# Optimization experiments

Hardware: AMD Instinct MI355X
Metric: run time of the kernel (lower is better)

## Reference

```python
import jax, jax.numpy as jnp
import numpy as np


def setup_inputs() -> dict:
    key = jax.random.key(0)
    k1, k2, k3, k4, k5 = jax.random.split(key, 5)
    B, D, H, W, C = 2, 16, 16, 16, 256
    x = jax.random.normal(k1, (B, D, H, W, C), dtype=jnp.float32)
    Wf = jax.random.normal(k2, (C, C // 4), dtype=jnp.float32) * (1.0 / np.sqrt(C))
    Wg = jax.random.normal(k3, (C, C // 4), dtype=jnp.float32) * (1.0 / np.sqrt(C))
    Wh = jax.random.normal(k4, (C, C), dtype=jnp.float32) * (1.0 / np.sqrt(C))
    gamma = jax.random.normal(k5, (1,), dtype=jnp.float32) * 0.1
    return {"x": x, "Wf": Wf, "Wg": Wg, "Wh": Wh, "gamma": gamma}


def reference(x, Wf, Wg, Wh, gamma):
    B, D, H, W, C = x.shape
    N = D * H * W
    xf = x.reshape(B, N, C)  # hw_flatten of input (1x1x1 conv == per-position matmul)
    f = jnp.einsum('bnc,cf->bnf', xf, Wf)   # [B, N, C//4]
    g = jnp.einsum('bnc,cf->bnf', xf, Wg)   # [B, N, C//4]
    h = jnp.einsum('bnc,cf->bnf', xf, Wh)   # [B, N, C]
    s = jnp.einsum('bnf,bmf->bnm', g, f)    # g @ f^T, [B, N, N]
    beta = jax.nn.softmax(s, axis=-1)
    o = jnp.einsum('bnm,bmc->bnc', beta, h)  # [B, N, C]
    out = gamma * o.reshape(B, D, H, W, C) + x
    beta_out = beta.reshape(-1, D, H, W, 1)  # [B*N, D, H, W, 1] as in original
    return (out, beta_out)
```

## Files before the change

### kernel.cpp

```cpp
#include <hip/hip_runtime.h>

#define NPOS 4096
#define CDIM 256
#define FDIM 64

typedef short short8 __attribute__((ext_vector_type(8)));
typedef float f32x4 __attribute__((ext_vector_type(4)));

__device__ __forceinline__ unsigned short f2bf(float v) {
  unsigned u = __float_as_uint(v);
  unsigned r = (u + 0x7fffu + ((u >> 16) & 1u)) >> 16;
  return (unsigned short)r;
}
__device__ __forceinline__ float bf2f(unsigned short u) {
  return __uint_as_float((unsigned)u << 16);
}
__device__ __forceinline__ short8 as_s8(uint4 u) {
  return *reinterpret_cast<short8*>(&u);
}
__device__ __forceinline__ void gload_lds16(const void* g, void* l) {
  __builtin_amdgcn_global_load_lds(
      (const __attribute__((address_space(1))) unsigned int*)g,
      (__attribute__((address_space(3))) unsigned int*)l, 16, 0, 0);
}

__global__ __launch_bounds__(256) void proj_kernel(
    const float* __restrict__ x, const float* __restrict__ Wf,
    const float* __restrict__ Wg, const float* __restrict__ Wh,
    unsigned short* __restrict__ f_hi, unsigned short* __restrict__ f_lo,
    unsigned short* __restrict__ g_hi, unsigned short* __restrict__ g_lo,
    unsigned short* __restrict__ h_t, float* __restrict__ out) {
  __shared__ float xs[16][CDIM];
  const int row0 = blockIdx.x * 16;
  const int t = threadIdx.x;
  {
    const float4* xv = reinterpret_cast<const float4*>(x + (size_t)row0 * CDIM);
    float4* sv = reinterpret_cast<float4*>(&xs[0][0]);
    float4* ov = reinterpret_cast<float4*>(out + (size_t)row0 * CDIM);
#pragma unroll
    for (int i = 0; i < 4; ++i) {
      const float4 v = xv[t + 256 * i];
      sv[t + 256 * i] = v;
      ov[t + 256 * i] = v;
    }
  }
  __syncthreads();
  {
    float acc[16];
#pragma unroll
    for (int r = 0; r < 16; ++r) acc[r] = 0.f;
    for (int k = 0; k < CDIM; k += 4) {
      const float w0 = Wh[(size_t)(k + 0) * CDIM + t];
      const float w1 = Wh[(size_t)(k + 1) * CDIM + t];
      const float w2 = Wh[(size_t)(k + 2) * CDIM + t];
      const float w3 = Wh[(size_t)(k + 3) * CDIM + t];
#pragma unroll
      for (int r = 0; r < 16; ++r) {
        const float4 xv = *reinterpret_cast<const float4*>(&xs[r][k]);
        float a = acc[r];
        a = fmaf(xv.x, w0, a);
        a = fmaf(xv.y, w1, a);
        a = fmaf(xv.z, w2, a);
        a = fmaf(xv.w, w3, a);
        acc[r] = a;
      }
    }
    const int b = row0 >> 12;
    const int lr = row0 & (NPOS - 1);
    unsigned wd[8];
#pragma unroll
    for (int i = 0; i < 8; ++i)
      wd[i] = (unsigned)f2bf(acc[2 * i]) | ((unsigned)f2bf(acc[2 * i + 1]) << 16);
    uint4* base = reinterpret_cast<uint4*>(h_t + ((size_t)(b * CDIM + t)) * NPOS);
    const int m = t & 7;
    const int c0 = lr >> 3;
    base[c0 ^ m] = make_uint4(wd[0], wd[1], wd[2], wd[3]);
    base[(c0 + 1) ^ m] = make_uint4(wd[4], wd[5], wd[6], wd[7]);
  }
  {
    const int col = t & 63;
    const int rb = (t >> 6) * 4;
    const int colq = col >> 3, cwi = col & 7;
    float af[4] = {0.f, 0.f, 0.f, 0.f};
    float ag[4] = {0.f, 0.f, 0.f, 0.f};
    for (int k = 0; k < CDIM; k += 4) {
      const float wf0 = Wf[(size_t)(k + 0) * FDIM + col];
      const float wf1 = Wf[(size_t)(k + 1) * FDIM + col];
      const float wf2 = Wf[(size_t)(k + 2) * FDIM + col];
      const float wf3 = Wf[(size_t)(k + 3) * FDIM + col];
      const float wg0 = Wg[(size_t)(k + 0) * FDIM + col];
      const float wg1 = Wg[(size_t)(k + 1) * FDIM + col];
      const float wg2 = Wg[(size_t)(k + 2) * FDIM + col];
      const float wg3 = Wg[(size_t)(k + 3) * FDIM + col];
#pragma unroll
      for (int r = 0; r < 4; ++r) {
        const float4 xv = *reinterpret_cast<const float4*>(&xs[rb + r][k]);
        float a = af[r], bb = ag[r];
        a = fmaf(xv.x, wf0, a); a = fmaf(xv.y, wf1, a);
        a = fmaf(xv.z, wf2, a); a = fmaf(xv.w, wf3, a);
        bb = fmaf(xv.x, wg0, bb); bb = fmaf(xv.y, wg1, bb);
        bb = fmaf(xv.z, wg2, bb); bb = fmaf(xv.w, wg3, bb);
        af[r] = a; ag[r] = bb;
      }
    }
#pragma unroll
    for (int r = 0; r < 4; ++r) {
      const int row = row0 + rb + r;
      const int ph = ((colq ^ (row & 7)) << 3) | cwi;
      const size_t of = (size_t)row * FDIM + ph;
      const size_t og = (size_t)row * FDIM + col;
      const unsigned short fh = f2bf(af[r]);
      const unsigned short gh = f2bf(ag[r]);
      f_hi[of] = fh;
      f_lo[of] = f2bf(af[r] - bf2f(fh));
      g_hi[og] = gh;
      g_lo[og] = f2bf(ag[r] - bf2f(gh));
    }
  }
}

__global__ __launch_bounds__(1024, 4) void qk_l_kernel(
    const unsigned short* __restrict__ f_hi, const unsigned short* __restrict__ f_lo,
    const unsigned short* __restrict__ g_hi, const unsigned short* __restrict__ g_lo,
    unsigned short* __restrict__ Pws, float* __restrict__ lrow) {
  __shared__ uint4 Fh[2][256][8];
  __shared__ uint4 Fl[2][256][8];
  __shared__ float partl[16][32];

  const int wg = blockIdx.x;
  const int wgid = (wg & 7) * 32 + (wg >> 3);
  const int b = wgid >> 7;
  const int row0 = (wgid & 127) * 32;
  const int t = threadIdx.x;
  const int w = t >> 6;
  const int l = t & 63;
  const int lr = l & 15;
  const int lk = l >> 4;

  short8 gh0[2], gl0[2], gh1[2], gl1[2];
  {
    const unsigned short* gH0 = g_hi + ((size_t)(b * NPOS + row0 + lr)) * FDIM + lk * 8;
    const unsigned short* gL0 = g_lo + ((size_t)(b * NPOS + row0 + lr)) * FDIM + lk * 8;
    const unsigned short* gH1 = gH0 + (size_t)16 * FDIM;
    const unsigned short* gL1 = gL0 + (size_t)16 * FDIM;
#pragma unroll
    for (int ks = 0; ks < 2; ++ks) {
      gh0[ks] = *reinterpret_cast<const short8*>(gH0 + ks * 32);
      gl0[ks] = *reinterpret_cast<const short8*>(gL0 + ks * 32);
      gh1[ks] = *reinterpret_cast<const short8*>(gH1 + ks * 32);
      gl1[ks] = *reinterpret_cast<const short8*>(gL1 + ks * 32);
    }
  }
  const unsigned short* fbh = f_hi + (size_t)b * NPOS * FDIM;
  const unsigned short* fbl = f_lo + (size_t)b * NPOS * FDIM;
  unsigned short* prow0 = Pws + (size_t)(b * NPOS + row0 + lr) * NPOS;
  unsigned short* prow1 = prow0 + (size_t)16 * NPOS;
  const int rsw = lr & 7;
  float lsum0 = 0.f, lsum1 = 0.f;

#define STAGEA(buf, tile)                                                      \
  do {                                                                         \
    _Pragma("unroll")                                                          \
    for (int j = 0; j < 2; ++j) {                                              \
      const int slot_ = j * 1024 + t;                                          \
      const int row_ = slot_ >> 3, ch_ = slot_ & 7;                            \
      gload_lds16(fbh + (size_t)((tile) * 256 + row_) * FDIM + ch_ * 8,        \
                  (char*)&Fh[buf][0][0] + (size_t)slot_ * 16);                 \
      gload_lds16(fbl + (size_t)((tile) * 256 + row_) * FDIM + ch_ * 8,        \
                  (char*)&Fl[buf][0][0] + (size_t)slot_ * 16);                 \
    }                                                                          \
  } while (0)

  STAGEA(0, 0);
  asm volatile("s_waitcnt vmcnt(0) lgkmcnt(0)\ns_barrier" ::: "memory");

  const int rrA = w * 16 + lr;
  const int fsw = rrA & 7;
  int buf = 0;
  for (int tile = 0; tile < 16; ++tile) {
    if (tile < 15) STAGEA(buf ^ 1, tile + 1);
    __builtin_amdgcn_sched_barrier(0);
    const uint4 h0 = Fh[buf][rrA][lk ^ fsw];
    const uint4 h1 = Fh[buf][rrA][(lk + 4) ^ fsw];
    const uint4 q0 = Fl[buf][rrA][lk ^ fsw];
    const uint4 q1 = Fl[buf][rrA][(lk + 4) ^ fsw];
    {
      f32x4 acca = {0.f, 0.f, 0.f, 0.f};
      f32x4 accb = {0.f, 0.f, 0.f, 0.f};
      acca = __builtin_amdgcn_mfma_f32_16x16x32_bf16(as_s8(h0), gh0[0], acca, 0, 0, 0);
      accb = __builtin_amdgcn_mfma_f32_16x16x32_bf16(as_s8(h0), gl0[0], accb, 0, 0, 0);
      acca = __builtin_amdgcn_mfma_f32_16x16x32_bf16(as_s8(q0), gh0[0], acca, 0, 0, 0);
      accb = __builtin_amdgcn_mfma_f32_16x16x32_bf16(as_s8(h1), gh0[1], accb, 0, 0, 0);
      acca = __builtin_amdgcn_mfma_f32_16x16x32_bf16(as_s8(q1), gh0[1], acca, 0, 0, 0);
      accb = __builtin_amdgcn_mfma_f32_16x16x32_bf16(as_s8(h1), gl0[1], accb, 0, 0, 0);
      const f32x4 acc = acca + accb;
      const int cq = tile * 256 + w * 16 + lk * 4;
      const float e0 = __expf(acc[0]);
      const float e1 = __expf(acc[1]);
      const float e2 = __expf(acc[2]);
      const float e3 = __expf(acc[3]);
      lsum0 += (e0 + e1) + (e2 + e3);
      uint2 pk;
      pk.x = (unsigned)f2bf(e0) | ((unsigned)f2bf(e1) << 16);
      pk.y = (unsigned)f2bf(e2) | ((unsigned)f2bf(e3) << 16);
      const int sidx = (((cq >> 3) ^ rsw) << 3) | (cq & 7);
      *reinterpret_cast<uint2*>(prow0 + sidx) = pk;
    }
    {
      f32x4 acca = {0.f, 0.f, 0.f, 0.f};
      f32x4 accb = {0.f, 0.f, 0.f, 0.f};
      acca = __builtin_amdgcn_mfma_f32_16x16x32_bf16(as_s8(h0), gh1[0], acca, 0, 0, 0);
      accb = __builtin_amdgcn_mfma_f32_16x16x32_bf16(as_s8(h0), gl1[0], accb, 0, 0, 0);
      acca = __builtin_amdgcn_mfma_f32_16x16x32_bf16(as_s8(q0), gh1[0], acca, 0, 0, 0);
      accb = __builtin_amdgcn_mfma_f32_16x16x32_bf16(as_s8(h1), gh1[1], accb, 0, 0, 0);
      acca = __builtin_amdgcn_mfma_f32_16x16x32_bf16(as_s8(q1), gh1[1], acca, 0, 0, 0);
      accb = __builtin_amdgcn_mfma_f32_16x16x32_bf16(as_s8(h1), gl1[1], accb, 0, 0, 0);
      const f32x4 acc = acca + accb;
      const int cq = tile * 256 + w * 16 + lk * 4;
      const float e0 = __expf(acc[0]);
      const float e1 = __expf(acc[1]);
      const float e2 = __expf(acc[2]);
      const float e3 = __expf(acc[3]);
      lsum1 += (e0 + e1) + (e2 + e3);
      uint2 pk;
      pk.x = (unsigned)f2bf(e0) | ((unsigned)f2bf(e1) << 16);
      pk.y = (unsigned)f2bf(e2) | ((unsigned)f2bf(e3) << 16);
      const int sidx = (((cq >> 3) ^ rsw) << 3) | (cq & 7);
      *reinterpret_cast<uint2*>(prow1 + sidx) = pk;
    }
    asm volatile("s_waitcnt vmcnt(2) lgkmcnt(0)\ns_barrier" ::: "memory");
    buf ^= 1;
  }
#undef STAGEA

  lsum0 += __shfl_xor(lsum0, 16);
  lsum0 += __shfl_xor(lsum0, 32);
  lsum1 += __shfl_xor(lsum1, 16);
  lsum1 += __shfl_xor(lsum1, 32);
  if (l < 16) {
    partl[w][l] = lsum0;
    partl[w][16 + l] = lsum1;
  }
  __syncthreads();
  if (t < 32) {
    float s = 0.f;
#pragma unroll
    for (int q = 0; q < 16; ++q) s += partl[q][t];
    lrow[(size_t)b * NPOS + row0 + t] = s;
  }
}

__global__ __launch_bounds__(1024, 4) void pv_split_kernel(
    const unsigned short* __restrict__ h_t, const unsigned short* __restrict__ Pws,
    const float* __restrict__ lrow, const float* __restrict__ gamma,
    float* __restrict__ beta, float* __restrict__ out) {
  __shared__ uint4 Ab[2][64][8];
  __shared__ uint4 Bb[2][256][8];
  __shared__ float linvB[64];

  const int wg = blockIdx.x;
  const int wgid = (wg & 7) * 32 + (wg >> 3);
  const int b = wgid >> 7;
  const int khalf = (wgid >> 6) & 1;
  const int row0 = (wgid & 63) * 64;
  const int t = threadIdx.x;
  const int w = t >> 6;
  const int l = t & 63;
  const int lr = l & 15;
  const int lk = l >> 4;

  if (t < 64) linvB[t] = __frcp_rn(lrow[(size_t)b * NPOS + row0 + t]);

  const size_t hoff = (size_t)b * CDIM * NPOS;
  const unsigned short* Pb = Pws + (size_t)(b * NPOS + row0) * NPOS;
  const int kbase = khalf * 256;

#define STAGEB(bufi, kt)                                                        \
  do {                                                                          \
    _Pragma("unroll")                                                           \
    for (int j = 0; j < 2; ++j) {                                               \
      const int slot_ = j * 1024 + t;                                           \
      const int col_ = slot_ >> 3, ch_ = slot_ & 7;                             \
      const unsigned short* g_ = h_t + hoff + (size_t)col_ * NPOS +             \
                                 (size_t)(kbase + (kt) * 8 + ch_) * 8;          \
      gload_lds16(g_, (char*)&Bb[bufi][0][0] + (size_t)slot_ * 16);             \
    }                                                                           \
    if (t < 512) {                                                              \
      const int row_ = t >> 3, ch_ = t & 7;                                     \
      const unsigned short* g_ = Pb + (size_t)row_ * NPOS +                     \
                                 (size_t)(kbase + (kt) * 8 + ch_) * 8;          \
      gload_lds16(g_, (char*)&Ab[bufi][0][0] + (size_t)t * 16);                 \
    }                                                                           \
  } while (0)

  f32x4 acc0 = {0.f, 0.f, 0.f, 0.f}, acc1 = {0.f, 0.f, 0.f, 0.f};
  f32x4 acc2 = {0.f, 0.f, 0.f, 0.f}, acc3 = {0.f, 0.f, 0.f, 0.f};
  const int wrB = w & 3;
  const int wcB = w >> 2;
  const int arB = wrB * 16 + lr;
  const int c0 = wcB * 64 + lr;
  const int c1 = c0 + 16;
  const int c2 = c0 + 32;
  const int c3 = c0 + 48;
  const int brow = t >> 4;
  const int jj = t & 15;

  STAGEB(0, 0);
  asm volatile("s_waitcnt vmcnt(0) lgkmcnt(0)\ns_barrier" ::: "memory");
  const float il_brow = linvB[brow];

  int buf = 0;
  for (int kt = 0; kt < 32; ++kt) {
    if (kt < 31) STAGEB(buf ^ 1, kt + 1);
    __builtin_amdgcn_sched_barrier(0);
    {
      const uint4 a0 = Ab[buf][arB][lk ^ (arB & 7)];
      const uint4 a1 = Ab[buf][arB][(4 + lk) ^ (arB & 7)];
      const uint4 b00 = Bb[buf][c0][lk ^ (c0 & 7)];
      const uint4 b01 = Bb[buf][c1][lk ^ (c1 & 7)];
      const uint4 b02 = Bb[buf][c2][lk ^ (c2 & 7)];
      const uint4 b03 = Bb[buf][c3][lk ^ (c3 & 7)];
      acc0 = __builtin_amdgcn_mfma_f32_16x16x32_bf16(as_s8(a0), as_s8(b00), acc0, 0, 0, 0);
      acc1 = __builtin_amdgcn_mfma_f32_16x16x32_bf16(as_s8(a0), as_s8(b01), acc1, 0, 0, 0);
      acc2 = __builtin_amdgcn_mfma_f32_16x16x32_bf16(as_s8(a0), as_s8(b02), acc2, 0, 0, 0);
      acc3 = __builtin_amdgcn_mfma_f32_16x16x32_bf16(as_s8(a0), as_s8(b03), acc3, 0, 0, 0);
      const uint4 b10 = Bb[buf][c0][(4 + lk) ^ (c0 & 7)];
      const uint4 b11 = Bb[buf][c1][(4 + lk) ^ (c1 & 7)];
      const uint4 b12 = Bb[buf][c2][(4 + lk) ^ (c2 & 7)];
      const uint4 b13 = Bb[buf][c3][(4 + lk) ^ (c3 & 7)];
      acc0 = __builtin_amdgcn_mfma_f32_16x16x32_bf16(as_s8(a1), as_s8(b10), acc0, 0, 0, 0);
      acc1 = __builtin_amdgcn_mfma_f32_16x16x32_bf16(as_s8(a1), as_s8(b11), acc1, 0, 0, 0);
      acc2 = __builtin_amdgcn_mfma_f32_16x16x32_bf16(as_s8(a1), as_s8(b12), acc2, 0, 0, 0);
      acc3 = __builtin_amdgcn_mfma_f32_16x16x32_bf16(as_s8(a1), as_s8(b13), acc3, 0, 0, 0);
    }
    {
      const uint4 u4 = Ab[buf][brow][(jj >> 1) ^ (brow & 7)];
      const uint2 u = (jj & 1) ? make_uint2(u4.z, u4.w) : make_uint2(u4.x, u4.y);
      float4 v;
      v.x = bf2f((unsigned short)(u.x & 0xffffu)) * il_brow;
      v.y = bf2f((unsigned short)(u.x >> 16)) * il_brow;
      v.z = bf2f((unsigned short)(u.y & 0xffffu)) * il_brow;
      v.w = bf2f((unsigned short)(u.y >> 16)) * il_brow;
      *reinterpret_cast<float4*>(beta + (size_t)(b * NPOS + row0 + brow) * NPOS +
                                 khalf * 2048 + kt * 64 + jj * 4) = v;
    }
    asm volatile("s_waitcnt vmcnt(1) lgkmcnt(0)\ns_barrier" ::: "memory");
    buf ^= 1;
  }
#undef STAGEB

  const float gam = gamma[0];
#pragma unroll
  for (int r = 0; r < 4; ++r) {
    const int lrr = wrB * 16 + lk * 4 + r;
    const int orow = row0 + lrr;
    const float sc = gam * linvB[lrr];
    float* o = out + ((size_t)b * NPOS + orow) * CDIM + wcB * 64 + lr;
    atomicAdd(o, sc * acc0[r]);
    atomicAdd(o + 16, sc * acc1[r]);
    atomicAdd(o + 32, sc * acc2[r]);
    atomicAdd(o + 48, sc * acc3[r]);
  }
}

__global__ __launch_bounds__(1024, 4) void attn_fused_kernel(
    const unsigned short* __restrict__ f_hi, const unsigned short* __restrict__ f_lo,
    const unsigned short* __restrict__ g_hi, const unsigned short* __restrict__ g_lo,
    const unsigned short* __restrict__ h_t, const float* __restrict__ x,
    const float* __restrict__ gamma, float* __restrict__ beta,
    float* __restrict__ out) {
  __shared__ __align__(16) char shraw[110592];
  __shared__ float partl[16][16];
  __shared__ float linvs[32];
  uint4 (*Fh)[128][8] = reinterpret_cast<uint4(*)[128][8]>(shraw);
  uint4 (*Fl)[128][8] = reinterpret_cast<uint4(*)[128][8]>(shraw + 32768);
  uint4 (*Ab)[32][8] = reinterpret_cast<uint4(*)[32][8]>(shraw);
  uint4 (*Bb)[256][8] = reinterpret_cast<uint4(*)[256][8]>(shraw + 12288);

  const int wg = blockIdx.x;
  const int wgid = (wg & 7) * 32 + (wg >> 3);
  const int b = wgid >> 7;
  const int row0 = (wgid & 127) * 32;
  const int t = threadIdx.x;
  const int w = t >> 6;
  const int l = t & 63;
  const int lr = l & 15;
  const int lk = l >> 4;

  const int wr = w >> 3;
  const int wq = w & 7;
  const int arow = row0 + wr * 16 + lr;
  short8 gh[2], gl[2];
  {
    const unsigned short* gH = g_hi + ((size_t)(b * NPOS + arow)) * FDIM + lk * 8;
    const unsigned short* gL = g_lo + ((size_t)(b * NPOS + arow)) * FDIM + lk * 8;
#pragma unroll
    for (int ks = 0; ks < 2; ++ks) {
      gh[ks] = *reinterpret_cast<const short8*>(gH + ks * 32);
      gl[ks] = *reinterpret_cast<const short8*>(gL + ks * 32);
    }
  }
  const unsigned short* fbh = f_hi + (size_t)b * NPOS * FDIM;
  const unsigned short* fbl = f_lo + (size_t)b * NPOS * FDIM;
  unsigned short* Pb = (unsigned short*)(beta + (size_t)b * NPOS * NPOS);
  unsigned short* prow = Pb + (size_t)arow * (2 * NPOS) + NPOS;
  const int rsw = lr & 7;
  float lsum = 0.f;
  const int srow_ = t >> 3, sch_ = t & 7;

#define STAGEA(buf, tile)                                                      \
  do {                                                                         \
    const int tr_ = (tile) * 128 + srow_;                                      \
    gload_lds16(fbh + (size_t)tr_ * FDIM + sch_ * 8,                           \
                (char*)&Fh[buf][0][0] + (size_t)t * 16);                       \
    gload_lds16(fbl + (size_t)tr_ * FDIM + sch_ * 8,                           \
                (char*)&Fl[buf][0][0] + (size_t)t * 16);                       \
  } while (0)

  STAGEA(0, 0);
  asm volatile("s_waitcnt vmcnt(0) lgkmcnt(0)\ns_barrier" ::: "memory");

  const int rrA = wq * 16 + lr;
  const int fsw = rrA & 7;
  int buf = 0;
  for (int tile = 0; tile < 32; ++tile) {
    if (tile < 31) STAGEA(buf ^ 1, tile + 1);
    __builtin_amdgcn_sched_barrier(0);
    const uint4 h0 = Fh[buf][rrA][lk ^ fsw];
    const uint4 h1 = Fh[buf][rrA][(lk + 4) ^ fsw];
    const uint4 q0 = Fl[buf][rrA][lk ^ fsw];
    const uint4 q1 = Fl[buf][rrA][(lk + 4) ^ fsw];
    f32x4 acca = {0.f, 0.f, 0.f, 0.f};
    f32x4 accb = {0.f, 0.f, 0.f, 0.f};
    acca = __builtin_amdgcn_mfma_f32_16x16x32_bf16(as_s8(h0), gh[0], acca, 0, 0, 0);
    accb = __builtin_amdgcn_mfma_f32_16x16x32_bf16(as_s8(h0), gl[0], accb, 0, 0, 0);
    acca = __builtin_amdgcn_mfma_f32_16x16x32_bf16(as_s8(q0), gh[0], acca, 0, 0, 0);
    accb = __builtin_amdgcn_mfma_f32_16x16x32_bf16(as_s8(h1), gh[1], accb, 0, 0, 0);
    acca = __builtin_amdgcn_mfma_f32_16x16x32_bf16(as_s8(q1), gh[1], acca, 0, 0, 0);
    accb = __builtin_amdgcn_mfma_f32_16x16x32_bf16(as_s8(h1), gl[1], accb, 0, 0, 0);
    const f32x4 acc = acca + accb;
    const int cq = tile * 128 + wq * 16 + lk * 4;
    const float e0 = __expf(acc[0]);
    const float e1 = __expf(acc[1]);
    const float e2 = __expf(acc[2]);
    const float e3 = __expf(acc[3]);
    lsum += (e0 + e1) + (e2 + e3);
    uint2 pk;
    pk.x = (unsigned)f2bf(e0) | ((unsigned)f2bf(e1) << 16);
    pk.y = (unsigned)f2bf(e2) | ((unsigned)f2bf(e3) << 16);
    const int sidx = (((cq >> 3) ^ rsw) << 3) | (cq & 7);
    *reinterpret_cast<uint2*>(prow + sidx) = pk;
    asm volatile("s_waitcnt vmcnt(1) lgkmcnt(0)\ns_barrier" ::: "memory");
    buf ^= 1;
  }
#undef STAGEA

  lsum += __shfl_xor(lsum, 16);
  lsum += __shfl_xor(lsum, 32);
  if (l < 16) partl[w][l] = lsum;
  __syncthreads();
  if (t < 32) {
    const int half = t >> 4;
    float s = 0.f;
#pragma unroll
    for (int q = 0; q < 8; ++q) s += partl[half * 8 + q][t & 15];
    linvs[t] = __frcp_rn(s);
  }
  asm volatile("s_waitcnt vmcnt(0) lgkmcnt(0)\ns_barrier" ::: "memory");

  const size_t hoff = (size_t)b * CDIM * NPOS;
  const unsigned short* Pub = (const unsigned short*)(beta + (size_t)b * NPOS * NPOS);

#define STAGEB(bufi, kt)                                                        \
  do {                                                                          \
    {                                                                           \
      const int slot_ = w * 128 + l;                                            \
      const unsigned short* g_ = h_t + hoff + (size_t)(slot_ >> 3) * NPOS +     \
                                 (size_t)((kt) * 8 + (slot_ & 7)) * 8;          \
      gload_lds16(g_, (unsigned short*)&Bb[bufi][0][0] + (size_t)(w * 128) * 8);\
    }                                                                           \
    {                                                                           \
      const int slot_ = w * 128 + 64 + l;                                       \
      const unsigned short* g_ = h_t + hoff + (size_t)(slot_ >> 3) * NPOS +     \
                                 (size_t)((kt) * 8 + (slot_ & 7)) * 8;          \
      gload_lds16(g_, (unsigned short*)&Bb[bufi][0][0] +                        \
                          (size_t)(w * 128 + 64) * 8);                          \
    }                                                                           \
    if (t < 256) {                                                              \
      const unsigned short* g_ = Pub + (size_t)(row0 + (t >> 3)) * (2 * NPOS) + \
                                 NPOS + (size_t)((kt) * 8 + (t & 7)) * 8;       \
      gload_lds16(g_, (unsigned short*)&Ab[bufi][0][0] + (size_t)(w * 64) * 8); \
    }                                                                           \
  } while (0)

  f32x4 acc0 = {0.f, 0.f, 0.f, 0.f}, acc1 = {0.f, 0.f, 0.f, 0.f};
  const int wrB = w & 1;
  const int wcB = w >> 1;
  const int arB = wrB * 16 + lr;
  const int c0 = wcB * 32 + lr;
  const int c1 = c0 + 16;
  const int brow = t >> 5;
  const int jj = t & 31;
  const float il_brow = linvs[brow];

  STAGEB(0, 0);
  asm volatile("s_waitcnt vmcnt(0) lgkmcnt(0)\ns_barrier" ::: "memory");

  buf = 0;
  for (int kt = 0; kt < 64; ++kt) {
    if (kt < 63) STAGEB(buf ^ 1, kt + 1);
    __builtin_amdgcn_sched_barrier(0);
    {
      const uint4 a0 = Ab[buf][arB][lk ^ (arB & 7)];
      const uint4 a1 = Ab[buf][arB][(4 + lk) ^ (arB & 7)];
      const uint4 b00 = Bb[buf][c0][lk ^ (c0 & 7)];
      const uint4 b01 = Bb[buf][c1][lk ^ (c1 & 7)];
      const uint4 b10 = Bb[buf][c0][(4 + lk) ^ (c0 & 7)];
      const uint4 b11 = Bb[buf][c1][(4 + lk) ^ (c1 & 7)];
      acc0 = __builtin_amdgcn_mfma_f32_16x16x32_bf16(as_s8(a0), as_s8(b00), acc0, 0, 0, 0);
      acc1 = __builtin_amdgcn_mfma_f32_16x16x32_bf16(as_s8(a0), as_s8(b01), acc1, 0, 0, 0);
      acc0 = __builtin_amdgcn_mfma_f32_16x16x32_bf16(as_s8(a1), as_s8(b10), acc0, 0, 0, 0);
      acc1 = __builtin_amdgcn_mfma_f32_16x16x32_bf16(as_s8(a1), as_s8(b11), acc1, 0, 0, 0);
    }
    {
      const unsigned* arow_ = reinterpret_cast<const unsigned*>(&Ab[buf][brow][0]);
      const unsigned u = arow_[(((jj >> 2) ^ (brow & 7)) << 2) | (jj & 3)];
      float2 v;
      v.x = bf2f((unsigned short)(u & 0xffffu)) * il_brow;
      v.y = bf2f((unsigned short)(u >> 16)) * il_brow;
      *reinterpret_cast<float2*>(beta + (size_t)(b * NPOS + row0 + brow) * NPOS +
                                 (size_t)kt * 64 + jj * 2) = v;
    }
    asm volatile("s_waitcnt vmcnt(1) lgkmcnt(0)\ns_barrier" ::: "memory");
    buf ^= 1;
  }
#undef STAGEB

  const float gam = gamma[0];
#pragma unroll
  for (int r = 0; r < 4; ++r) {
    const int lrr = wrB * 16 + lk * 4 + r;
    const int orow = row0 + lrr;
    const float sc = gam * linvs[lrr];
    const size_t i0 = ((size_t)b * NPOS + orow) * CDIM + wcB * 32 + lr;
    out[i0] = fmaf(sc, acc0[r], x[i0]);
    out[i0 + 16] = fmaf(sc, acc1[r], x[i0 + 16]);
  }
}

extern "C" void kernel_launch(void* const* d_in, const int* in_sizes, int n_in,
                              void* d_out, int out_size, void* d_ws, size_t ws_size,
                              hipStream_t stream) {
  (void)in_sizes; (void)n_in; (void)out_size;
  const float* x = (const float*)d_in[0];
  const float* Wf = (const float*)d_in[1];
  const float* Wg = (const float*)d_in[2];
  const float* Wh = (const float*)d_in[3];
  const float* gamma = (const float*)d_in[4];

  float* out = (float*)d_out;
  float* beta = out + (size_t)2 * NPOS * CDIM;

  unsigned short* h_t = (unsigned short*)d_ws;
  unsigned short* f_hi = h_t + (size_t)2 * CDIM * NPOS;
  unsigned short* f_lo = f_hi + (size_t)2 * NPOS * FDIM;
  unsigned short* g_hi = f_lo + (size_t)2 * NPOS * FDIM;
  unsigned short* g_lo = g_hi + (size_t)2 * NPOS * FDIM;
  float* lrow = (float*)(g_lo + (size_t)2 * NPOS * FDIM);
  unsigned short* Pws = (unsigned short*)(lrow + 2 * NPOS);

  const size_t need = ((char*)(Pws + (size_t)2 * NPOS * NPOS)) - (char*)d_ws;

  hipLaunchKernelGGL(proj_kernel, dim3(2 * NPOS / 16), dim3(256), 0, stream,
                     x, Wf, Wg, Wh, f_hi, f_lo, g_hi, g_lo, h_t, out);
  if (ws_size >= need) {
    hipLaunchKernelGGL(qk_l_kernel, dim3(256), dim3(1024), 0, stream,
                       f_hi, f_lo, g_hi, g_lo, Pws, lrow);
    hipLaunchKernelGGL(pv_split_kernel, dim3(256), dim3(1024), 0, stream,
                       h_t, Pws, lrow, gamma, beta, out);
  } else {
    hipLaunchKernelGGL(attn_fused_kernel, dim3(256), dim3(1024), 0, stream,
                       f_hi, f_lo, g_hi, g_lo, h_t, x, gamma, beta, out);
  }
}
```

Baseline: 125.7 us.

## Retile PV split kernel to 128-row blocks with four-way K split

Changes the PV kernel tiling so each workgroup handles 128 query rows against a quarter of the key range, instead of 64 rows against half. Each staged h tile is now reused by twice as many rows, and each wave computes eight accumulators instead of four, which cuts global traffic for h per unit of work. The cost is twice as many atomic partial-sum adds into the output, plus higher register and LDS use per block. The waitcnt is adjusted because each iteration now issues two beta stores.

```diff
diff --git a/kernel.cpp b/kernel.cpp
--- a/kernel.cpp
+++ b/kernel.cpp
@@ -254,26 +254,26 @@
     const unsigned short* __restrict__ h_t, const unsigned short* __restrict__ Pws,
     const float* __restrict__ lrow, const float* __restrict__ gamma,
     float* __restrict__ beta, float* __restrict__ out) {
-  __shared__ uint4 Ab[2][64][8];
+  __shared__ uint4 Ab[2][128][8];
   __shared__ uint4 Bb[2][256][8];
-  __shared__ float linvB[64];
+  __shared__ float linvB[128];
 
   const int wg = blockIdx.x;
   const int wgid = (wg & 7) * 32 + (wg >> 3);
   const int b = wgid >> 7;
-  const int khalf = (wgid >> 6) & 1;
-  const int row0 = (wgid & 63) * 64;
+  const int kq = (wgid >> 5) & 3;
+  const int row0 = (wgid & 31) * 128;
   const int t = threadIdx.x;
   const int w = t >> 6;
   const int l = t & 63;
   const int lr = l & 15;
   const int lk = l >> 4;
 
-  if (t < 64) linvB[t] = __frcp_rn(lrow[(size_t)b * NPOS + row0 + t]);
+  if (t < 128) linvB[t] = __frcp_rn(lrow[(size_t)b * NPOS + row0 + t]);
 
   const size_t hoff = (size_t)b * CDIM * NPOS;
   const unsigned short* Pb = Pws + (size_t)(b * NPOS + row0) * NPOS;
-  const int kbase = khalf * 256;
+  const int kbase = kq * 128;
 
 #define STAGEB(bufi, kt)                                                        \
   do {                                                                          \
@@ -285,7 +285,7 @@
                                  (size_t)(kbase + (kt) * 8 + ch_) * 8;          \
       gload_lds16(g_, (char*)&Bb[bufi][0][0] + (size_t)slot_ * 16);             \
     }                                                                           \
-    if (t < 512) {                                                              \
+    {                                                                           \
       const int row_ = t >> 3, ch_ = t & 7;                                     \
       const unsigned short* g_ = Pb + (size_t)row_ * NPOS +                     \
                                  (size_t)(kbase + (kt) * 8 + ch_) * 8;          \
@@ -293,47 +293,45 @@
     }                                                                           \
   } while (0)
 
-  f32x4 acc0 = {0.f, 0.f, 0.f, 0.f}, acc1 = {0.f, 0.f, 0.f, 0.f};
-  f32x4 acc2 = {0.f, 0.f, 0.f, 0.f}, acc3 = {0.f, 0.f, 0.f, 0.f};
-  const int wrB = w & 3;
-  const int wcB = w >> 2;
+  f32x4 acc[8];
+#pragma unroll
+  for (int c = 0; c < 8; ++c) acc[c] = (f32x4){0.f, 0.f, 0.f, 0.f};
+  const int wrB = w & 7;
+  const int wcB = w >> 3;
   const int arB = wrB * 16 + lr;
-  const int c0 = wcB * 64 + lr;
-  const int c1 = c0 + 16;
-  const int c2 = c0 + 32;
-  const int c3 = c0 + 48;
-  const int brow = t >> 4;
-  const int jj = t & 15;
+  const int cbase = wcB * 128 + lr;
+  const int brow = t >> 3;
+  const int jjb = t & 7;
 
   STAGEB(0, 0);
   asm volatile("s_waitcnt vmcnt(0) lgkmcnt(0)\ns_barrier" ::: "memory");
   const float il_brow = linvB[brow];
 
   int buf = 0;
-  for (int kt = 0; kt < 32; ++kt) {
-    if (kt < 31) STAGEB(buf ^ 1, kt + 1);
+  for (int kt = 0; kt < 16; ++kt) {
+    if (kt < 15) STAGEB(buf ^ 1, kt + 1);
     __builtin_amdgcn_sched_barrier(0);
     {
       const uint4 a0 = Ab[buf][arB][lk ^ (arB & 7)];
       const uint4 a1 = Ab[buf][arB][(4 + lk) ^ (arB & 7)];
-      const uint4 b00 = Bb[buf][c0][lk ^ (c0 & 7)];
-      const uint4 b01 = Bb[buf][c1][lk ^ (c1 & 7)];
-      const uint4 b02 = Bb[buf][c2][lk ^ (c2 & 7)];
-      const uint4 b03 = Bb[buf][c3][lk ^ (c3 & 7)];
-      acc0 = __builtin_amdgcn_mfma_f32_16x16x32_bf16(as_s8(a0), as_s8(b00), acc0, 0, 0, 0);
-      acc1 = __builtin_amdgcn_mfma_f32_16x16x32_bf16(as_s8(a0), as_s8(b01), acc1, 0, 0, 0);
-      acc2 = __builtin_amdgcn_mfma_f32_16x16x32_bf16(as_s8(a0), as_s8(b02), acc2, 0, 0, 0);
-      acc3 = __builtin_amdgcn_mfma_f32_16x16x32_bf16(as_s8(a0), as_s8(b03), acc3, 0, 0, 0);
-      const uint4 b10 = Bb[buf][c0][(4 + lk) ^ (c0 & 7)];
-      const uint4 b11 = Bb[buf][c1][(4 + lk) ^ (c1 & 7)];
-      const uint4 b12 = Bb[buf][c2][(4 + lk) ^ (c2 & 7)];
-      const uint4 b13 = Bb[buf][c3][(4 + lk) ^ (c3 & 7)];
-      acc0 = __builtin_amdgcn_mfma_f32_16x16x32_bf16(as_s8(a1), as_s8(b10), acc0, 0, 0, 0);
-      acc1 = __builtin_amdgcn_mfma_f32_16x16x32_bf16(as_s8(a1), as_s8(b11), acc1, 0, 0, 0);
-      acc2 = __builtin_amdgcn_mfma_f32_16x16x32_bf16(as_s8(a1), as_s8(b12), acc2, 0, 0, 0);
-      acc3 = __builtin_amdgcn_mfma_f32_16x16x32_bf16(as_s8(a1), as_s8(b13), acc3, 0, 0, 0);
-    }
-    {
+#pragma unroll
+      for (int c = 0; c < 8; ++c) {
+        const int cc = cbase + 16 * c;
+        const uint4 b0 = Bb[buf][cc][lk ^ (cc & 7)];
+        acc[c] = __builtin_amdgcn_mfma_f32_16x16x32_bf16(as_s8(a0), as_s8(b0),
+                                                         acc[c], 0, 0, 0);
+      }
+#pragma unroll
+      for (int c = 0; c < 8; ++c) {
+        const int cc = cbase + 16 * c;
+        const uint4 b1 = Bb[buf][cc][(4 + lk) ^ (cc & 7)];
+        acc[c] = __builtin_amdgcn_mfma_f32_16x16x32_bf16(as_s8(a1), as_s8(b1),
+                                                         acc[c], 0, 0, 0);
+      }
+    }
+#pragma unroll
+    for (int q = 0; q < 2; ++q) {
+      const int jj = jjb + q * 8;
       const uint4 u4 = Ab[buf][brow][(jj >> 1) ^ (brow & 7)];
       const uint2 u = (jj & 1) ? make_uint2(u4.z, u4.w) : make_uint2(u4.x, u4.y);
       float4 v;
@@ -342,9 +340,9 @@
       v.z = bf2f((unsigned short)(u.y & 0xffffu)) * il_brow;
       v.w = bf2f((unsigned short)(u.y >> 16)) * il_brow;
       *reinterpret_cast<float4*>(beta + (size_t)(b * NPOS + row0 + brow) * NPOS +
-                                 khalf * 2048 + kt * 64 + jj * 4) = v;
-    }
-    asm volatile("s_waitcnt vmcnt(1) lgkmcnt(0)\ns_barrier" ::: "memory");
+                                 kq * 1024 + kt * 64 + jj * 4) = v;
+    }
+    asm volatile("s_waitcnt vmcnt(2) lgkmcnt(0)\ns_barrier" ::: "memory");
     buf ^= 1;
   }
 #undef STAGEB
@@ -355,11 +353,9 @@
     const int lrr = wrB * 16 + lk * 4 + r;
     const int orow = row0 + lrr;
     const float sc = gam * linvB[lrr];
-    float* o = out + ((size_t)b * NPOS + orow) * CDIM + wcB * 64 + lr;
-    atomicAdd(o, sc * acc0[r]);
-    atomicAdd(o + 16, sc * acc1[r]);
-    atomicAdd(o + 32, sc * acc2[r]);
-    atomicAdd(o + 48, sc * acc3[r]);
+    float* o = out + ((size_t)b * NPOS + orow) * CDIM + cbase;
+#pragma unroll
+    for (int c = 0; c < 8; ++c) atomicAdd(o + 16 * c, sc * acc[c][r]);
   }
 }
 
```

Result: slower. 135.5 us (+7.9%).
